# Performance work log

Measured on AMD Instinct MI355X. Metric: run time of the kernel, lower is better.

## Reference

```python
import jax, jax.numpy as jnp
from jax import lax
import numpy as np

MAX_VAL = 255.0
LEVELS = 5
MS_WEIGHTS = np.array([0.0448, 0.2856, 0.3001, 0.2363, 0.1333], dtype=np.float32)


def _gaussian_window(window_size: int, sigma: float) -> jnp.ndarray:
    # 1D gaussian -> outer product -> [1, 1, ws, ws] conv kernel (channel=1 depthwise)
    x = np.arange(window_size, dtype=np.float64)
    g = np.exp(-((x - window_size // 2) ** 2) / (2.0 * sigma ** 2))
    g = (g / g.sum()).astype(np.float32)
    w2d = np.outer(g, g)
    return jnp.asarray(w2d[None, None, :, :])


def _conv_same(x, win, pad):
    return lax.conv_general_dilated(
        x, win, window_strides=(1, 1), padding=[(pad, pad), (pad, pad)],
        dimension_numbers=('NCHW', 'OIHW', 'NCHW'))


def _ssim_level(img1, img2):
    _, _, w, h = img1.shape
    window_size = min(w, h, 11)
    sigma = 1.5 * window_size / 11
    win = _gaussian_window(window_size, sigma)
    pad = window_size // 2

    mu1 = _conv_same(img1, win, pad)
    mu2 = _conv_same(img2, win, pad)
    mu1_sq = mu1 * mu1
    mu2_sq = mu2 * mu2
    mu1_mu2 = mu1 * mu2
    sigma1_sq = _conv_same(img1 * img1, win, pad) - mu1_sq
    sigma2_sq = _conv_same(img2 * img2, win, pad) - mu2_sq
    sigma12 = _conv_same(img1 * img2, win, pad) - mu1_mu2

    C1 = (0.01 * MAX_VAL) ** 2
    C2 = (0.03 * MAX_VAL) ** 2
    V1 = 2.0 * sigma12 + C2
    V2 = sigma1_sq + sigma2_sq + C2
    ssim_map = (2.0 * mu1_mu2 + C1) * V1 / ((mu1_sq + mu2_sq + C1) * V2)
    mcs_map = V1 / V2
    return ssim_map.mean(), mcs_map.mean()


def _avg_pool2(x):
    b, c, h, w = x.shape
    return x.reshape(b, c, h // 2, 2, w // 2, 2).mean(axis=(3, 5))


def _ms_ssim(img1, img2):
    msssim = []
    mcs = []
    for _ in range(LEVELS):
        s, m = _ssim_level(img1, img2)
        msssim.append(s)
        mcs.append(m)
        img1 = _avg_pool2(img1)
        img2 = _avg_pool2(img2)
    weight = jnp.asarray(MS_WEIGHTS)
    mcs = jnp.stack(mcs)
    value = jnp.prod(mcs[:LEVELS - 1] ** weight[:LEVELS - 1]) * msssim[-1] ** weight[LEVELS - 1]
    return jnp.clip(value / 2.0, 0.0, 1.0)


def setup_inputs() -> dict:
    key = jax.random.key(0)
    k1, k2 = jax.random.split(key)
    shape = (16, 1, 512, 512)
    img1 = jax.random.uniform(k1, shape, dtype=jnp.float32)
    img2 = jax.random.uniform(k2, shape, dtype=jnp.float32)
    return {"img1": img1, "img2": img2}


def reference(img1, img2):
    return _ms_ssim(img1, img2)
```

## Files before the change

### kernel.cpp

```cpp
#include <hip/hip_runtime.h>
#include <math.h>


#define WS 11
#define TW 64
#define TH 32
#define SROWS 42
#define HSTRIDE 68

__global__ __launch_bounds__(256) void ssim_level_kernel(
    const float* __restrict__ img1, const float* __restrict__ img2,
    int H, int W,
    float* __restrict__ pool1, float* __restrict__ pool2,
    float* __restrict__ partials)
{
    __shared__ float hS[SROWS * HSTRIDE];
    __shared__ float hD[SROWS * HSTRIDE];
    __shared__ float hS2[SROWS * HSTRIDE];
    __shared__ float hD2[SROWS * HSTRIDE];
    __shared__ float wgs[WS];
    __shared__ float red[2][4];

    const int tid = threadIdx.x;

    if (tid == 0) {
        double g[WS]; double sum = 0.0;
        for (int i = 0; i < WS; ++i) {
            double d = (double)(i - 5);
            g[i] = exp(-(d * d) / 4.5);
            sum += g[i];
        }
        for (int i = 0; i < WS; ++i) wgs[i] = (float)(g[i] / sum);
    }
    __syncthreads();

    float w[WS];
#pragma unroll
    for (int j = 0; j < WS; ++j) w[j] = wgs[j];

    const int bx = blockIdx.x, by = blockIdx.y, b = blockIdx.z;
    const int x0 = bx * TW, y0 = by * TH;
    const float* p1 = img1 + (size_t)b * H * W;
    const float* p2 = img2 + (size_t)b * H * W;

#pragma unroll 1
    for (int t = tid; t < SROWS * 16; t += 256) {
        int r = t >> 4, xg = t & 15;
        int gy = y0 - 5 + r;
        int gxb = x0 - 8 + 4 * xg;
        float fs[20], fd[20];
        if (gy >= 0 && gy < H) {
            const float* r1p = p1 + (size_t)gy * W;
            const float* r2p = p2 + (size_t)gy * W;
#pragma unroll
            for (int k = 0; k < 5; ++k) {
                int gx = gxb + 4 * k;
                float4 a = make_float4(0.f, 0.f, 0.f, 0.f);
                float4 c = make_float4(0.f, 0.f, 0.f, 0.f);
                if (gx >= 0 && gx + 3 < W) {
                    a = *(const float4*)(r1p + gx);
                    c = *(const float4*)(r2p + gx);
                } else if (gx + 3 >= 0 && gx < W) {
                    float t1[4] = {0.f, 0.f, 0.f, 0.f};
                    float t2[4] = {0.f, 0.f, 0.f, 0.f};
#pragma unroll
                    for (int u = 0; u < 4; ++u) {
                        int gxx = gx + u;
                        if (gxx >= 0 && gxx < W) { t1[u] = r1p[gxx]; t2[u] = r2p[gxx]; }
                    }
                    a = make_float4(t1[0], t1[1], t1[2], t1[3]);
                    c = make_float4(t2[0], t2[1], t2[2], t2[3]);
                }
                fs[4 * k]     = a.x + c.x;  fd[4 * k]     = a.x - c.x;
                fs[4 * k + 1] = a.y + c.y;  fd[4 * k + 1] = a.y - c.y;
                fs[4 * k + 2] = a.z + c.z;  fd[4 * k + 2] = a.z - c.z;
                fs[4 * k + 3] = a.w + c.w;  fd[4 * k + 3] = a.w - c.w;
            }
        } else {
#pragma unroll
            for (int k = 0; k < 20; ++k) { fs[k] = 0.f; fd[k] = 0.f; }
        }
        float qs[14], qd[14];
#pragma unroll
        for (int k = 0; k < 14; ++k) {
            qs[k] = fs[k + 3] * fs[k + 3];
            qd[k] = fd[k + 3] * fd[k + 3];
        }
        float oS[4], oD[4], oS2[4], oD2[4];
#pragma unroll
        for (int c = 0; c < 4; ++c) {
            float aS = 0.f, aD = 0.f, aS2 = 0.f, aD2 = 0.f;
#pragma unroll
            for (int j = 0; j < WS; ++j) {
                float wj = w[j];
                aS  = fmaf(wj, fs[3 + c + j], aS);
                aD  = fmaf(wj, fd[3 + c + j], aD);
                aS2 = fmaf(wj, qs[c + j], aS2);
                aD2 = fmaf(wj, qd[c + j], aD2);
            }
            oS[c] = aS; oD[c] = aD; oS2[c] = aS2; oD2[c] = aD2;
        }
        int ho = r * HSTRIDE + 4 * xg;
        *(float4*)&hS[ho]  = make_float4(oS[0], oS[1], oS[2], oS[3]);
        *(float4*)&hD[ho]  = make_float4(oD[0], oD[1], oD[2], oD[3]);
        *(float4*)&hS2[ho] = make_float4(oS2[0], oS2[1], oS2[2], oS2[3]);
        *(float4*)&hD2[ho] = make_float4(oD2[0], oD2[1], oD2[2], oD2[3]);
    }

    if (pool1 != nullptr) {
        int pc = tid & 15, pr = tid >> 4;
        int Hp = H >> 1, Wp = W >> 1;
        int gy = y0 + 2 * pr, gx = x0 + 4 * pc;
        const float* r1a = p1 + (size_t)gy * W + gx;
        const float* r1b = r1a + W;
        const float* r2a = p2 + (size_t)gy * W + gx;
        const float* r2b = r2a + W;
        float4 a0 = *(const float4*)r1a, a1 = *(const float4*)r1b;
        float4 c0 = *(const float4*)r2a, c1 = *(const float4*)r2b;
        float2 px = make_float2(0.25f * (a0.x + a0.y + a1.x + a1.y),
                                0.25f * (a0.z + a0.w + a1.z + a1.w));
        float2 py = make_float2(0.25f * (c0.x + c0.y + c1.x + c1.y),
                                0.25f * (c0.z + c0.w + c1.z + c1.w));
        size_t o = ((size_t)b * Hp + (by * (TH / 2) + pr)) * Wp + (bx * (TW / 2) + 2 * pc);
        *(float2*)(pool1 + o) = px;
        *(float2*)(pool2 + o) = py;
    }

    __syncthreads();

    const int x = tid & 15;
    const int g = tid >> 4;
    float accS[2][4], accD[2][4], accS2[2][4], accD2[2][4];
#pragma unroll
    for (int rr = 0; rr < 2; ++rr)
#pragma unroll
        for (int c = 0; c < 4; ++c) {
            accS[rr][c] = 0.f; accD[rr][c] = 0.f;
            accS2[rr][c] = 0.f; accD2[rr][c] = 0.f;
        }

#pragma unroll
    for (int r = 0; r < 12; ++r) {
        int ho = (2 * g + r) * HSTRIDE + 4 * x;
        float4 vS  = *(const float4*)&hS[ho];
        float4 vD  = *(const float4*)&hD[ho];
        float4 vS2 = *(const float4*)&hS2[ho];
        float4 vD2 = *(const float4*)&hD2[ho];
        float lS[4] = {vS.x, vS.y, vS.z, vS.w};
        float lD[4] = {vD.x, vD.y, vD.z, vD.w};
        float lS2[4] = {vS2.x, vS2.y, vS2.z, vS2.w};
        float lD2[4] = {vD2.x, vD2.y, vD2.z, vD2.w};
        if (r < 11) {
            float wv = w[r];
#pragma unroll
            for (int c = 0; c < 4; ++c) {
                accS[0][c]  = fmaf(wv, lS[c],  accS[0][c]);
                accD[0][c]  = fmaf(wv, lD[c],  accD[0][c]);
                accS2[0][c] = fmaf(wv, lS2[c], accS2[0][c]);
                accD2[0][c] = fmaf(wv, lD2[c], accD2[0][c]);
            }
        }
        if (r >= 1) {
            float wv = w[r - 1];
#pragma unroll
            for (int c = 0; c < 4; ++c) {
                accS[1][c]  = fmaf(wv, lS[c],  accS[1][c]);
                accD[1][c]  = fmaf(wv, lD[c],  accD[1][c]);
                accS2[1][c] = fmaf(wv, lS2[c], accS2[1][c]);
                accD2[1][c] = fmaf(wv, lD2[c], accD2[1][c]);
            }
        }
    }

    const float C1 = 6.5025f;
    const float C2 = 58.5225f;
    const int Hv = min(TH, H - y0);
    const int Wv = min(TW, W - x0);
    float sacc = 0.f, macc = 0.f;
#pragma unroll
    for (int rr = 0; rr < 2; ++rr) {
        int row = 2 * g + rr;
#pragma unroll
        for (int c = 0; c < 4; ++c) {
            float ms = accS[rr][c], md = accD[rr][c];
            float es = accS2[rr][c], ed = accD2[rr][c];
            float ms2 = ms * ms, md2 = md * md;
            float a  = 0.5f * (ms2 - md2);
            float bb = 0.5f * (ms2 + md2);
            float pq = 0.5f * (es - ed);
            float qq = 0.5f * (es + ed);
            float V1 = (pq - a) + C2;
            float V2 = (qq - bb) + C2;
            float num = a + C1;
            float den = bb + C1;
            float inv = 1.0f / (den * V2);
            float sv = num * V1 * inv;
            float mv = V1 * den * inv;
            if (row < Hv && (4 * x + c) < Wv) { sacc += sv; macc += mv; }
        }
    }

#pragma unroll
    for (int o = 32; o > 0; o >>= 1) {
        sacc += __shfl_down(sacc, o);
        macc += __shfl_down(macc, o);
    }
    int wave = tid >> 6, lane = tid & 63;
    if (lane == 0) { red[0][wave] = sacc; red[1][wave] = macc; }
    __syncthreads();
    if (tid == 0) {
        float s = red[0][0] + red[0][1] + red[0][2] + red[0][3];
        float m = red[1][0] + red[1][1] + red[1][2] + red[1][3];
        size_t linear = ((size_t)blockIdx.z * gridDim.y + blockIdx.y) * gridDim.x + blockIdx.x;
        partials[2 * linear] = s;
        partials[2 * linear + 1] = m;
    }
}

__global__ __launch_bounds__(256) void finalize_kernel(
    const float* __restrict__ partials, float* __restrict__ out)
{
    __shared__ float lvl_s[5], lvl_m[5];
    __shared__ float red[2][4];
    const int nb[5] = {2048, 512, 128, 32, 16};
    const int off[5] = {0, 2048, 2560, 2688, 2720};
    const float npix[5] = {16.f * 512 * 512, 16.f * 256 * 256, 16.f * 128 * 128,
                           16.f * 64 * 64, 16.f * 32 * 32};
    const int tid = threadIdx.x;

    for (int l = 0; l < 5; ++l) {
        float s = 0.f, m = 0.f;
        for (int i = tid; i < nb[l]; i += 256) {
            s += partials[2 * (off[l] + i)];
            m += partials[2 * (off[l] + i) + 1];
        }
#pragma unroll
        for (int o = 32; o > 0; o >>= 1) {
            s += __shfl_down(s, o);
            m += __shfl_down(m, o);
        }
        int wave = tid >> 6, lane = tid & 63;
        if (lane == 0) { red[0][wave] = s; red[1][wave] = m; }
        __syncthreads();
        if (tid == 0) {
            lvl_s[l] = (red[0][0] + red[0][1] + red[0][2] + red[0][3]) / npix[l];
            lvl_m[l] = (red[1][0] + red[1][1] + red[1][2] + red[1][3]) / npix[l];
        }
        __syncthreads();
    }

    if (tid == 0) {
        const float w[5] = {0.0448f, 0.2856f, 0.3001f, 0.2363f, 0.1333f};
        float v = powf(lvl_m[0], w[0]) * powf(lvl_m[1], w[1]) * powf(lvl_m[2], w[2]) *
                  powf(lvl_m[3], w[3]) * powf(lvl_s[4], w[4]);
        v *= 0.5f;
        v = fminf(fmaxf(v, 0.f), 1.f);
        out[0] = v;
    }
}

extern "C" void kernel_launch(void* const* d_in, const int* in_sizes, int n_in,
                              void* d_out, int out_size, void* d_ws, size_t ws_size,
                              hipStream_t stream) {
    const float* img1 = (const float*)d_in[0];
    const float* img2 = (const float*)d_in[1];
    float* out = (float*)d_out;

    const int B = 16;

    float* wsf = (float*)d_ws;
    float* partials = wsf;
    float* p = wsf + 5472;
    float* p1_l1 = p; p += (size_t)B * 256 * 256;
    float* p2_l1 = p; p += (size_t)B * 256 * 256;
    float* p1_l2 = p; p += (size_t)B * 128 * 128;
    float* p2_l2 = p; p += (size_t)B * 128 * 128;
    float* p1_l3 = p; p += (size_t)B * 64 * 64;
    float* p2_l3 = p; p += (size_t)B * 64 * 64;
    float* p1_l4 = p; p += (size_t)B * 32 * 32;
    float* p2_l4 = p; p += (size_t)B * 32 * 32;

    const int part_off[5] = {0, 2048, 2560, 2688, 2720};

    dim3 block(256);

    ssim_level_kernel<<<dim3(8, 16, B), block, 0, stream>>>(
        img1, img2, 512, 512, p1_l1, p2_l1, partials + 2 * part_off[0]);
    ssim_level_kernel<<<dim3(4, 8, B), block, 0, stream>>>(
        p1_l1, p2_l1, 256, 256, p1_l2, p2_l2, partials + 2 * part_off[1]);
    ssim_level_kernel<<<dim3(2, 4, B), block, 0, stream>>>(
        p1_l2, p2_l2, 128, 128, p1_l3, p2_l3, partials + 2 * part_off[2]);
    ssim_level_kernel<<<dim3(1, 2, B), block, 0, stream>>>(
        p1_l3, p2_l3, 64, 64, p1_l4, p2_l4, partials + 2 * part_off[3]);
    ssim_level_kernel<<<dim3(1, 1, B), block, 0, stream>>>(
        p1_l4, p2_l4, 32, 32, nullptr, nullptr, partials + 2 * part_off[4]);

    finalize_kernel<<<1, block, 0, stream>>>(partials, out);
}
```

Measured before the change: 147.6 us.

## Build full pyramid in one pass and run all SSIM levels in one launch

A new kernel computes all four downsampled pyramid levels from 64x64 tiles of the full-resolution images, chaining the 2x2 pools through shared memory. A single SSIM kernel then handles every level, mapping a flat block index to a level and tile, so the five serial per-level launches with their tail effects become one launch where the small levels fill in beside the large one. Gaussian weights are now computed per thread in float instead of by one thread in double followed by a barrier. The cost is an extra full read of the input images for pooling and slight float differences in the weights.

```diff
diff --git a/kernel.cpp b/kernel.cpp
--- a/kernel.cpp
+++ b/kernel.cpp
@@ -8,40 +8,128 @@
 #define SROWS 42
 #define HSTRIDE 68
 
-__global__ __launch_bounds__(256) void ssim_level_kernel(
+__device__ __forceinline__ void gauss_weights(float* w) {
+    float s = 0.f;
+#pragma unroll
+    for (int j = 0; j < WS; ++j) {
+        float d = (float)(j - 5);
+        float e = expf(-d * d / 4.5f);
+        w[j] = e;
+        s += e;
+    }
+    float inv = 1.f / s;
+#pragma unroll
+    for (int j = 0; j < WS; ++j) w[j] *= inv;
+}
+
+__global__ __launch_bounds__(256) void pool_all_kernel(
     const float* __restrict__ img1, const float* __restrict__ img2,
-    int H, int W,
-    float* __restrict__ pool1, float* __restrict__ pool2,
+    float* __restrict__ l1a, float* __restrict__ l1b,
+    float* __restrict__ l2a, float* __restrict__ l2b,
+    float* __restrict__ l3a, float* __restrict__ l3b,
+    float* __restrict__ l4a, float* __restrict__ l4b)
+{
+    __shared__ float buf[64 * 68];
+    __shared__ float pl1[32 * 36];
+    __shared__ float pl2[16 * 20];
+    __shared__ float pl3[8 * 12];
+    const int tid = threadIdx.x;
+    const int rx = blockIdx.x, ry = blockIdx.y, b = blockIdx.z;
+    const int gx0 = rx * 64, gy0 = ry * 64;
+
+#pragma unroll 1
+    for (int q = 0; q < 2; ++q) {
+        const float* src = (q == 0 ? img1 : img2) + (size_t)b * 512 * 512;
+        float* d1 = (q == 0 ? l1a : l1b) + (size_t)b * 256 * 256;
+        float* d2 = (q == 0 ? l2a : l2b) + (size_t)b * 128 * 128;
+        float* d3 = (q == 0 ? l3a : l3b) + (size_t)b * 64 * 64;
+        float* d4 = (q == 0 ? l4a : l4b) + (size_t)b * 32 * 32;
+        if (q) __syncthreads();
+        for (int t = tid; t < 1024; t += 256) {
+            int r = t >> 4, c4 = t & 15;
+            float4 v = *(const float4*)(src + (size_t)(gy0 + r) * 512 + gx0 + 4 * c4);
+            *(float4*)&buf[r * 68 + 4 * c4] = v;
+        }
+        __syncthreads();
+        for (int t = tid; t < 1024; t += 256) {
+            int r = t >> 5, c = t & 31;
+            const float* p = &buf[(2 * r) * 68 + 2 * c];
+            float v = 0.25f * ((p[0] + p[1]) + (p[68] + p[69]));
+            pl1[r * 36 + c] = v;
+            d1[(size_t)(32 * ry + r) * 256 + 32 * rx + c] = v;
+        }
+        __syncthreads();
+        {
+            int r = tid >> 4, c = tid & 15;
+            const float* p = &pl1[(2 * r) * 36 + 2 * c];
+            float v = 0.25f * ((p[0] + p[1]) + (p[36] + p[37]));
+            pl2[r * 20 + c] = v;
+            d2[(size_t)(16 * ry + r) * 128 + 16 * rx + c] = v;
+        }
+        __syncthreads();
+        if (tid < 64) {
+            int r = tid >> 3, c = tid & 7;
+            const float* p = &pl2[(2 * r) * 20 + 2 * c];
+            float v = 0.25f * ((p[0] + p[1]) + (p[20] + p[21]));
+            pl3[r * 12 + c] = v;
+            d3[(size_t)(8 * ry + r) * 64 + 8 * rx + c] = v;
+        }
+        __syncthreads();
+        if (tid < 16) {
+            int r = tid >> 2, c = tid & 3;
+            const float* p = &pl3[(2 * r) * 12 + 2 * c];
+            float v = 0.25f * ((p[0] + p[1]) + (p[12] + p[13]));
+            d4[(size_t)(4 * ry + r) * 32 + 4 * rx + c] = v;
+        }
+    }
+}
+
+__global__ __launch_bounds__(256) void ssim_fused_kernel(
+    const float* __restrict__ img1, const float* __restrict__ img2,
+    const float* __restrict__ l1a, const float* __restrict__ l1b,
+    const float* __restrict__ l2a, const float* __restrict__ l2b,
+    const float* __restrict__ l3a, const float* __restrict__ l3b,
+    const float* __restrict__ l4a, const float* __restrict__ l4b,
     float* __restrict__ partials)
 {
     __shared__ float hS[SROWS * HSTRIDE];
     __shared__ float hD[SROWS * HSTRIDE];
     __shared__ float hS2[SROWS * HSTRIDE];
     __shared__ float hD2[SROWS * HSTRIDE];
-    __shared__ float wgs[WS];
     __shared__ float red[2][4];
 
     const int tid = threadIdx.x;
-
-    if (tid == 0) {
-        double g[WS]; double sum = 0.0;
-        for (int i = 0; i < WS; ++i) {
-            double d = (double)(i - 5);
-            g[i] = exp(-(d * d) / 4.5);
-            sum += g[i];
-        }
-        for (int i = 0; i < WS; ++i) wgs[i] = (float)(g[i] / sum);
-    }
-    __syncthreads();
+    const int lin = blockIdx.x;
+
+    int level, base;
+    if (lin < 2048)      { level = 0; base = 0; }
+    else if (lin < 2560) { level = 1; base = 2048; }
+    else if (lin < 2688) { level = 2; base = 2560; }
+    else if (lin < 2720) { level = 3; base = 2688; }
+    else                 { level = 4; base = 2720; }
+    const int Wt[5]   = {512, 256, 128, 64, 32};
+    const int ntxl[5] = {3, 2, 1, 0, 0};
+    const int ntyl[5] = {4, 3, 2, 1, 0};
+    const int W = Wt[level], H = W;
+    const int li = lin - base;
+    const int tx = li & ((1 << ntxl[level]) - 1);
+    const int rem = li >> ntxl[level];
+    const int ty = rem & ((1 << ntyl[level]) - 1);
+    const int b = rem >> ntyl[level];
+
+    const float* ip1; const float* ip2;
+    if (level == 0)      { ip1 = img1; ip2 = img2; }
+    else if (level == 1) { ip1 = l1a; ip2 = l1b; }
+    else if (level == 2) { ip1 = l2a; ip2 = l2b; }
+    else if (level == 3) { ip1 = l3a; ip2 = l3b; }
+    else                 { ip1 = l4a; ip2 = l4b; }
+    const float* p1 = ip1 + (size_t)b * H * W;
+    const float* p2 = ip2 + (size_t)b * H * W;
+
+    const int x0 = tx * TW, y0 = ty * TH;
 
     float w[WS];
-#pragma unroll
-    for (int j = 0; j < WS; ++j) w[j] = wgs[j];
-
-    const int bx = blockIdx.x, by = blockIdx.y, b = blockIdx.z;
-    const int x0 = bx * TW, y0 = by * TH;
-    const float* p1 = img1 + (size_t)b * H * W;
-    const float* p2 = img2 + (size_t)b * H * W;
+    gauss_weights(w);
 
 #pragma unroll 1
     for (int t = tid; t < SROWS * 16; t += 256) {
@@ -106,26 +194,6 @@
         *(float4*)&hS2[ho] = make_float4(oS2[0], oS2[1], oS2[2], oS2[3]);
         *(float4*)&hD2[ho] = make_float4(oD2[0], oD2[1], oD2[2], oD2[3]);
     }
-
-    if (pool1 != nullptr) {
-        int pc = tid & 15, pr = tid >> 4;
-        int Hp = H >> 1, Wp = W >> 1;
-        int gy = y0 + 2 * pr, gx = x0 + 4 * pc;
-        const float* r1a = p1 + (size_t)gy * W + gx;
-        const float* r1b = r1a + W;
-        const float* r2a = p2 + (size_t)gy * W + gx;
-        const float* r2b = r2a + W;
-        float4 a0 = *(const float4*)r1a, a1 = *(const float4*)r1b;
-        float4 c0 = *(const float4*)r2a, c1 = *(const float4*)r2b;
-        float2 px = make_float2(0.25f * (a0.x + a0.y + a1.x + a1.y),
-                                0.25f * (a0.z + a0.w + a1.z + a1.w));
-        float2 py = make_float2(0.25f * (c0.x + c0.y + c1.x + c1.y),
-                                0.25f * (c0.z + c0.w + c1.z + c1.w));
-        size_t o = ((size_t)b * Hp + (by * (TH / 2) + pr)) * Wp + (bx * (TW / 2) + 2 * pc);
-        *(float2*)(pool1 + o) = px;
-        *(float2*)(pool2 + o) = py;
-    }
-
     __syncthreads();
 
     const int x = tid & 15;
@@ -211,9 +279,8 @@
     if (tid == 0) {
         float s = red[0][0] + red[0][1] + red[0][2] + red[0][3];
         float m = red[1][0] + red[1][1] + red[1][2] + red[1][3];
-        size_t linear = ((size_t)blockIdx.z * gridDim.y + blockIdx.y) * gridDim.x + blockIdx.x;
-        partials[2 * linear] = s;
-        partials[2 * linear + 1] = m;
+        partials[2 * lin] = s;
+        partials[2 * lin + 1] = m;
     }
 }
 
@@ -271,29 +338,22 @@
     float* wsf = (float*)d_ws;
     float* partials = wsf;
     float* p = wsf + 5472;
-    float* p1_l1 = p; p += (size_t)B * 256 * 256;
-    float* p2_l1 = p; p += (size_t)B * 256 * 256;
-    float* p1_l2 = p; p += (size_t)B * 128 * 128;
-    float* p2_l2 = p; p += (size_t)B * 128 * 128;
-    float* p1_l3 = p; p += (size_t)B * 64 * 64;
-    float* p2_l3 = p; p += (size_t)B * 64 * 64;
-    float* p1_l4 = p; p += (size_t)B * 32 * 32;
-    float* p2_l4 = p; p += (size_t)B * 32 * 32;
-
-    const int part_off[5] = {0, 2048, 2560, 2688, 2720};
+    float* l1a = p; p += (size_t)B * 256 * 256;
+    float* l1b = p; p += (size_t)B * 256 * 256;
+    float* l2a = p; p += (size_t)B * 128 * 128;
+    float* l2b = p; p += (size_t)B * 128 * 128;
+    float* l3a = p; p += (size_t)B * 64 * 64;
+    float* l3b = p; p += (size_t)B * 64 * 64;
+    float* l4a = p; p += (size_t)B * 32 * 32;
+    float* l4b = p; p += (size_t)B * 32 * 32;
 
     dim3 block(256);
 
-    ssim_level_kernel<<<dim3(8, 16, B), block, 0, stream>>>(
-        img1, img2, 512, 512, p1_l1, p2_l1, partials + 2 * part_off[0]);
-    ssim_level_kernel<<<dim3(4, 8, B), block, 0, stream>>>(
-        p1_l1, p2_l1, 256, 256, p1_l2, p2_l2, partials + 2 * part_off[1]);
-    ssim_level_kernel<<<dim3(2, 4, B), block, 0, stream>>>(
-        p1_l2, p2_l2, 128, 128, p1_l3, p2_l3, partials + 2 * part_off[2]);
-    ssim_level_kernel<<<dim3(1, 2, B), block, 0, stream>>>(
-        p1_l3, p2_l3, 64, 64, p1_l4, p2_l4, partials + 2 * part_off[3]);
-    ssim_level_kernel<<<dim3(1, 1, B), block, 0, stream>>>(
-        p1_l4, p2_l4, 32, 32, nullptr, nullptr, partials + 2 * part_off[4]);
+    pool_all_kernel<<<dim3(8, 8, B), block, 0, stream>>>(
+        img1, img2, l1a, l1b, l2a, l2b, l3a, l3b, l4a, l4b);
+
+    ssim_fused_kernel<<<dim3(2736), block, 0, stream>>>(
+        img1, img2, l1a, l1b, l2a, l2b, l3a, l3b, l4a, l4b, partials);
 
     finalize_kernel<<<1, block, 0, stream>>>(partials, out);
 }
```

Result: faster. 129.4 us (-12.3%).

## Fuse all MS-SSIM levels and finalize into one kernel with on-the-fly pooling

Applied to the files above, without the earlier changes.

Replaces the five per-level launches plus the finalize launch with a single grid. Each block picks its pyramid level from its linear index and recomputes the pooled pixels directly from the full-resolution images into shared memory, using a templated recursive average. The last block to finish, detected with an atomic counter, reduces all partials and writes the result. This removes launch overhead and the serial dependency between levels, at the cost of redundant reads for deep levels (up to 256 loads per pooled pixel at level 4), more shared memory per block, and a memset launch.

```diff
diff --git a/kernel.cpp b/kernel.cpp
--- a/kernel.cpp
+++ b/kernel.cpp
@@ -7,78 +7,192 @@
 #define TH 32
 #define SROWS 42
 #define HSTRIDE 68
-
-__global__ __launch_bounds__(256) void ssim_level_kernel(
+#define PSTRIDE 84
+#define NBLK 2736
+
+__device__ __forceinline__ void gauss_weights(float* w) {
+    float s = 0.f;
+#pragma unroll
+    for (int j = 0; j < WS; ++j) {
+        float d = (float)(j - 5);
+        float e = expf(-d * d / 4.5f);
+        w[j] = e;
+        s += e;
+    }
+    float inv = 1.f / s;
+#pragma unroll
+    for (int j = 0; j < WS; ++j) w[j] *= inv;
+}
+
+template<int L>
+__device__ __forceinline__ float poolT(const float* __restrict__ img, int y, int x) {
+    if constexpr (L == 0) {
+        return img[(y << 9) + x];
+    } else {
+        return 0.25f * ((poolT<L-1>(img, 2*y, 2*x)   + poolT<L-1>(img, 2*y, 2*x+1)) +
+                        (poolT<L-1>(img, 2*y+1, 2*x) + poolT<L-1>(img, 2*y+1, 2*x+1)));
+    }
+}
+
+__global__ __launch_bounds__(256) void msssim_all_kernel(
     const float* __restrict__ img1, const float* __restrict__ img2,
-    int H, int W,
-    float* __restrict__ pool1, float* __restrict__ pool2,
-    float* __restrict__ partials)
+    float* __restrict__ partials, unsigned int* __restrict__ counter,
+    float* __restrict__ out)
 {
     __shared__ float hS[SROWS * HSTRIDE];
     __shared__ float hD[SROWS * HSTRIDE];
     __shared__ float hS2[SROWS * HSTRIDE];
     __shared__ float hD2[SROWS * HSTRIDE];
-    __shared__ float wgs[WS];
+    __shared__ float pS[SROWS * PSTRIDE];
+    __shared__ float pD[SROWS * PSTRIDE];
     __shared__ float red[2][4];
+    __shared__ int lastflag;
 
     const int tid = threadIdx.x;
-
-    if (tid == 0) {
-        double g[WS]; double sum = 0.0;
-        for (int i = 0; i < WS; ++i) {
-            double d = (double)(i - 5);
-            g[i] = exp(-(d * d) / 4.5);
-            sum += g[i];
-        }
-        for (int i = 0; i < WS; ++i) wgs[i] = (float)(g[i] / sum);
-    }
-    __syncthreads();
+    const int lin = blockIdx.x;
+
+    int level, li;
+    if (lin < 16)       { level = 4; li = lin; }
+    else if (lin < 48)  { level = 3; li = lin - 16; }
+    else if (lin < 176) { level = 2; li = lin - 48; }
+    else if (lin < 688) { level = 1; li = lin - 176; }
+    else                { level = 0; li = lin - 688; }
+
+    const int ntxl[5] = {3, 2, 1, 0, 0};
+    const int ntyl[5] = {4, 3, 2, 1, 0};
+    const int W = 512 >> level;
+    const int tx = li & ((1 << ntxl[level]) - 1);
+    const int rem = li >> ntxl[level];
+    const int ty = rem & ((1 << ntyl[level]) - 1);
+    const int b = rem >> ntyl[level];
+    const int x0 = tx * TW, y0 = ty * TH;
+
+    const float* p1 = img1 + (size_t)b * 512 * 512;
+    const float* p2 = img2 + (size_t)b * 512 * 512;
 
     float w[WS];
-#pragma unroll
-    for (int j = 0; j < WS; ++j) w[j] = wgs[j];
-
-    const int bx = blockIdx.x, by = blockIdx.y, b = blockIdx.z;
-    const int x0 = bx * TW, y0 = by * TH;
-    const float* p1 = img1 + (size_t)b * H * W;
-    const float* p2 = img2 + (size_t)b * H * W;
-
+    gauss_weights(w);
+
+    if (level > 0) {
+        if (level == 1) {
+            for (int t = tid; t < SROWS * 80; t += 256) {
+                int r = t / 80, c = t - r * 80;
+                int gy = y0 - 5 + r, gx = x0 - 8 + c;
+                float vS = 0.f, vD = 0.f;
+                if ((unsigned)gy < (unsigned)W && (unsigned)gx < (unsigned)W) {
+                    float a = poolT<1>(p1, gy, gx);
+                    float bb = poolT<1>(p2, gy, gx);
+                    vS = a + bb; vD = a - bb;
+                }
+                pS[r * PSTRIDE + c] = vS;
+                pD[r * PSTRIDE + c] = vD;
+            }
+        } else if (level == 2) {
+            for (int t = tid; t < SROWS * 80; t += 256) {
+                int r = t / 80, c = t - r * 80;
+                int gy = y0 - 5 + r, gx = x0 - 8 + c;
+                float vS = 0.f, vD = 0.f;
+                if ((unsigned)gy < (unsigned)W && (unsigned)gx < (unsigned)W) {
+                    float a = poolT<2>(p1, gy, gx);
+                    float bb = poolT<2>(p2, gy, gx);
+                    vS = a + bb; vD = a - bb;
+                }
+                pS[r * PSTRIDE + c] = vS;
+                pD[r * PSTRIDE + c] = vD;
+            }
+        } else if (level == 3) {
+            for (int t = tid; t < SROWS * 80; t += 256) {
+                int r = t / 80, c = t - r * 80;
+                int gy = y0 - 5 + r, gx = x0 - 8 + c;
+                float vS = 0.f, vD = 0.f;
+                if ((unsigned)gy < (unsigned)W && (unsigned)gx < (unsigned)W) {
+                    float a = poolT<3>(p1, gy, gx);
+                    float bb = poolT<3>(p2, gy, gx);
+                    vS = a + bb; vD = a - bb;
+                }
+                pS[r * PSTRIDE + c] = vS;
+                pD[r * PSTRIDE + c] = vD;
+            }
+        } else {
+            for (int t = tid; t < SROWS * 80; t += 256) {
+                int r = t / 80, c = t - r * 80;
+                int gy = y0 - 5 + r, gx = x0 - 8 + c;
+                float vS = 0.f, vD = 0.f;
+                if ((unsigned)gy < (unsigned)W && (unsigned)gx < (unsigned)W) {
+                    float a = poolT<4>(p1, gy, gx);
+                    float bb = poolT<4>(p2, gy, gx);
+                    vS = a + bb; vD = a - bb;
+                }
+                pS[r * PSTRIDE + c] = vS;
+                pD[r * PSTRIDE + c] = vD;
+            }
+        }
+        __syncthreads();
+    }
+
+    const bool interior = (level == 0) && (x0 >= 8) && (x0 <= 440) &&
+                          (y0 >= 5) && (y0 <= 475);
 #pragma unroll 1
     for (int t = tid; t < SROWS * 16; t += 256) {
         int r = t >> 4, xg = t & 15;
-        int gy = y0 - 5 + r;
-        int gxb = x0 - 8 + 4 * xg;
         float fs[20], fd[20];
-        if (gy >= 0 && gy < H) {
-            const float* r1p = p1 + (size_t)gy * W;
-            const float* r2p = p2 + (size_t)gy * W;
+        if (level == 0) {
+            int gy = y0 - 5 + r;
+            int gxb = x0 - 8 + 4 * xg;
+            if (interior) {
+                const float* r1p = p1 + (size_t)gy * 512 + gxb;
+                const float* r2p = p2 + (size_t)gy * 512 + gxb;
+#pragma unroll
+                for (int k = 0; k < 5; ++k) {
+                    float4 a = *(const float4*)(r1p + 4 * k);
+                    float4 c = *(const float4*)(r2p + 4 * k);
+                    fs[4 * k]     = a.x + c.x;  fd[4 * k]     = a.x - c.x;
+                    fs[4 * k + 1] = a.y + c.y;  fd[4 * k + 1] = a.y - c.y;
+                    fs[4 * k + 2] = a.z + c.z;  fd[4 * k + 2] = a.z - c.z;
+                    fs[4 * k + 3] = a.w + c.w;  fd[4 * k + 3] = a.w - c.w;
+                }
+            } else if (gy >= 0 && gy < 512) {
+                const float* r1p = p1 + (size_t)gy * 512;
+                const float* r2p = p2 + (size_t)gy * 512;
+#pragma unroll
+                for (int k = 0; k < 5; ++k) {
+                    int gx = gxb + 4 * k;
+                    float4 a = make_float4(0.f, 0.f, 0.f, 0.f);
+                    float4 c = make_float4(0.f, 0.f, 0.f, 0.f);
+                    if (gx >= 0 && gx + 3 < 512) {
+                        a = *(const float4*)(r1p + gx);
+                        c = *(const float4*)(r2p + gx);
+                    } else if (gx + 3 >= 0 && gx < 512) {
+                        float t1[4] = {0.f, 0.f, 0.f, 0.f};
+                        float t2[4] = {0.f, 0.f, 0.f, 0.f};
+#pragma unroll
+                        for (int u = 0; u < 4; ++u) {
+                            int gxx = gx + u;
+                            if (gxx >= 0 && gxx < 512) { t1[u] = r1p[gxx]; t2[u] = r2p[gxx]; }
+                        }
+                        a = make_float4(t1[0], t1[1], t1[2], t1[3]);
+                        c = make_float4(t2[0], t2[1], t2[2], t2[3]);
+                    }
+                    fs[4 * k]     = a.x + c.x;  fd[4 * k]     = a.x - c.x;
+                    fs[4 * k + 1] = a.y + c.y;  fd[4 * k + 1] = a.y - c.y;
+                    fs[4 * k + 2] = a.z + c.z;  fd[4 * k + 2] = a.z - c.z;
+                    fs[4 * k + 3] = a.w + c.w;  fd[4 * k + 3] = a.w - c.w;
+                }
+            } else {
+#pragma unroll
+                for (int k = 0; k < 20; ++k) { fs[k] = 0.f; fd[k] = 0.f; }
+            }
+        } else {
+            int base = r * PSTRIDE + 4 * xg;
 #pragma unroll
             for (int k = 0; k < 5; ++k) {
-                int gx = gxb + 4 * k;
-                float4 a = make_float4(0.f, 0.f, 0.f, 0.f);
-                float4 c = make_float4(0.f, 0.f, 0.f, 0.f);
-                if (gx >= 0 && gx + 3 < W) {
-                    a = *(const float4*)(r1p + gx);
-                    c = *(const float4*)(r2p + gx);
-                } else if (gx + 3 >= 0 && gx < W) {
-                    float t1[4] = {0.f, 0.f, 0.f, 0.f};
-                    float t2[4] = {0.f, 0.f, 0.f, 0.f};
-#pragma unroll
-                    for (int u = 0; u < 4; ++u) {
-                        int gxx = gx + u;
-                        if (gxx >= 0 && gxx < W) { t1[u] = r1p[gxx]; t2[u] = r2p[gxx]; }
-                    }
-                    a = make_float4(t1[0], t1[1], t1[2], t1[3]);
-                    c = make_float4(t2[0], t2[1], t2[2], t2[3]);
-                }
-                fs[4 * k]     = a.x + c.x;  fd[4 * k]     = a.x - c.x;
-                fs[4 * k + 1] = a.y + c.y;  fd[4 * k + 1] = a.y - c.y;
-                fs[4 * k + 2] = a.z + c.z;  fd[4 * k + 2] = a.z - c.z;
-                fs[4 * k + 3] = a.w + c.w;  fd[4 * k + 3] = a.w - c.w;
-            }
-        } else {
-#pragma unroll
-            for (int k = 0; k < 20; ++k) { fs[k] = 0.f; fd[k] = 0.f; }
+                float4 a = *(const float4*)&pS[base + 4 * k];
+                float4 c = *(const float4*)&pD[base + 4 * k];
+                fs[4 * k]     = a.x;  fd[4 * k]     = c.x;
+                fs[4 * k + 1] = a.y;  fd[4 * k + 1] = c.y;
+                fs[4 * k + 2] = a.z;  fd[4 * k + 2] = c.z;
+                fs[4 * k + 3] = a.w;  fd[4 * k + 3] = c.w;
+            }
         }
         float qs[14], qd[14];
 #pragma unroll
@@ -106,26 +220,6 @@
         *(float4*)&hS2[ho] = make_float4(oS2[0], oS2[1], oS2[2], oS2[3]);
         *(float4*)&hD2[ho] = make_float4(oD2[0], oD2[1], oD2[2], oD2[3]);
     }
-
-    if (pool1 != nullptr) {
-        int pc = tid & 15, pr = tid >> 4;
-        int Hp = H >> 1, Wp = W >> 1;
-        int gy = y0 + 2 * pr, gx = x0 + 4 * pc;
-        const float* r1a = p1 + (size_t)gy * W + gx;
-        const float* r1b = r1a + W;
-        const float* r2a = p2 + (size_t)gy * W + gx;
-        const float* r2b = r2a + W;
-        float4 a0 = *(const float4*)r1a, a1 = *(const float4*)r1b;
-        float4 c0 = *(const float4*)r2a, c1 = *(const float4*)r2b;
-        float2 px = make_float2(0.25f * (a0.x + a0.y + a1.x + a1.y),
-                                0.25f * (a0.z + a0.w + a1.z + a1.w));
-        float2 py = make_float2(0.25f * (c0.x + c0.y + c1.x + c1.y),
-                                0.25f * (c0.z + c0.w + c1.z + c1.w));
-        size_t o = ((size_t)b * Hp + (by * (TH / 2) + pr)) * Wp + (bx * (TW / 2) + 2 * pc);
-        *(float2*)(pool1 + o) = px;
-        *(float2*)(pool2 + o) = py;
-    }
-
     __syncthreads();
 
     const int x = tid & 15;
@@ -174,7 +268,7 @@
 
     const float C1 = 6.5025f;
     const float C2 = 58.5225f;
-    const int Hv = min(TH, H - y0);
+    const int Hv = min(TH, W - y0);
     const int Wv = min(TW, W - x0);
     float sacc = 0.f, macc = 0.f;
 #pragma unroll
@@ -211,51 +305,62 @@
     if (tid == 0) {
         float s = red[0][0] + red[0][1] + red[0][2] + red[0][3];
         float m = red[1][0] + red[1][1] + red[1][2] + red[1][3];
-        size_t linear = ((size_t)blockIdx.z * gridDim.y + blockIdx.y) * gridDim.x + blockIdx.x;
-        partials[2 * linear] = s;
-        partials[2 * linear + 1] = m;
-    }
-}
-
-__global__ __launch_bounds__(256) void finalize_kernel(
-    const float* __restrict__ partials, float* __restrict__ out)
-{
-    __shared__ float lvl_s[5], lvl_m[5];
-    __shared__ float red[2][4];
-    const int nb[5] = {2048, 512, 128, 32, 16};
-    const int off[5] = {0, 2048, 2560, 2688, 2720};
-    const float npix[5] = {16.f * 512 * 512, 16.f * 256 * 256, 16.f * 128 * 128,
-                           16.f * 64 * 64, 16.f * 32 * 32};
-    const int tid = threadIdx.x;
-
-    for (int l = 0; l < 5; ++l) {
-        float s = 0.f, m = 0.f;
-        for (int i = tid; i < nb[l]; i += 256) {
-            s += partials[2 * (off[l] + i)];
-            m += partials[2 * (off[l] + i) + 1];
+        partials[2 * lin] = s;
+        partials[2 * lin + 1] = m;
+        __threadfence();
+        unsigned int old = __hip_atomic_fetch_add(counter, 1u, __ATOMIC_ACQ_REL,
+                                                  __HIP_MEMORY_SCOPE_AGENT);
+        lastflag = (old == NBLK - 1) ? 1 : 0;
+    }
+    __syncthreads();
+
+    if (lastflag) {
+        __threadfence();
+        const int offk[5] = {0, 16, 48, 176, 688};
+        const int endk[5] = {16, 48, 176, 688, NBLK};
+        float aS[5], aM[5];
+#pragma unroll
+        for (int k = 0; k < 5; ++k) {
+            float s = 0.f, m = 0.f;
+            for (int i = offk[k] + tid; i < endk[k]; i += 256) {
+                s += partials[2 * i];
+                m += partials[2 * i + 1];
+            }
+            aS[k] = s; aM[k] = m;
         }
 #pragma unroll
         for (int o = 32; o > 0; o >>= 1) {
-            s += __shfl_down(s, o);
-            m += __shfl_down(m, o);
-        }
-        int wave = tid >> 6, lane = tid & 63;
-        if (lane == 0) { red[0][wave] = s; red[1][wave] = m; }
+#pragma unroll
+            for (int k = 0; k < 5; ++k) {
+                aS[k] += __shfl_down(aS[k], o);
+                aM[k] += __shfl_down(aM[k], o);
+            }
+        }
+        if (lane == 0) {
+#pragma unroll
+            for (int k = 0; k < 5; ++k) {
+                pS[wave * 16 + k] = aS[k];
+                pS[wave * 16 + 8 + k] = aM[k];
+            }
+        }
         __syncthreads();
         if (tid == 0) {
-            lvl_s[l] = (red[0][0] + red[0][1] + red[0][2] + red[0][3]) / npix[l];
-            lvl_m[l] = (red[1][0] + red[1][1] + red[1][2] + red[1][3]) / npix[l];
-        }
-        __syncthreads();
-    }
-
-    if (tid == 0) {
-        const float w[5] = {0.0448f, 0.2856f, 0.3001f, 0.2363f, 0.1333f};
-        float v = powf(lvl_m[0], w[0]) * powf(lvl_m[1], w[1]) * powf(lvl_m[2], w[2]) *
-                  powf(lvl_m[3], w[3]) * powf(lvl_s[4], w[4]);
-        v *= 0.5f;
-        v = fminf(fmaxf(v, 0.f), 1.f);
-        out[0] = v;
+            const float npix[5] = {16384.f, 65536.f, 262144.f, 1048576.f, 4194304.f};
+            float ls[5], lm[5];
+#pragma unroll
+            for (int k = 0; k < 5; ++k) {
+                float s = pS[k] + pS[16 + k] + pS[32 + k] + pS[48 + k];
+                float m = pS[8 + k] + pS[24 + k] + pS[40 + k] + pS[56 + k];
+                ls[k] = s / npix[k];
+                lm[k] = m / npix[k];
+            }
+            const float wt[5] = {0.0448f, 0.2856f, 0.3001f, 0.2363f, 0.1333f};
+            float v = powf(lm[4], wt[0]) * powf(lm[3], wt[1]) * powf(lm[2], wt[2]) *
+                      powf(lm[1], wt[3]) * powf(ls[0], wt[4]);
+            v *= 0.5f;
+            v = fminf(fmaxf(v, 0.f), 1.f);
+            out[0] = v;
+        }
     }
 }
 
@@ -266,34 +371,12 @@
     const float* img2 = (const float*)d_in[1];
     float* out = (float*)d_out;
 
-    const int B = 16;
-
     float* wsf = (float*)d_ws;
     float* partials = wsf;
-    float* p = wsf + 5472;
-    float* p1_l1 = p; p += (size_t)B * 256 * 256;
-    float* p2_l1 = p; p += (size_t)B * 256 * 256;
-    float* p1_l2 = p; p += (size_t)B * 128 * 128;
-    float* p2_l2 = p; p += (size_t)B * 128 * 128;
-    float* p1_l3 = p; p += (size_t)B * 64 * 64;
-    float* p2_l3 = p; p += (size_t)B * 64 * 64;
-    float* p1_l4 = p; p += (size_t)B * 32 * 32;
-    float* p2_l4 = p; p += (size_t)B * 32 * 32;
-
-    const int part_off[5] = {0, 2048, 2560, 2688, 2720};
-
-    dim3 block(256);
-
-    ssim_level_kernel<<<dim3(8, 16, B), block, 0, stream>>>(
-        img1, img2, 512, 512, p1_l1, p2_l1, partials + 2 * part_off[0]);
-    ssim_level_kernel<<<dim3(4, 8, B), block, 0, stream>>>(
-        p1_l1, p2_l1, 256, 256, p1_l2, p2_l2, partials + 2 * part_off[1]);
-    ssim_level_kernel<<<dim3(2, 4, B), block, 0, stream>>>(
-        p1_l2, p2_l2, 128, 128, p1_l3, p2_l3, partials + 2 * part_off[2]);
-    ssim_level_kernel<<<dim3(1, 2, B), block, 0, stream>>>(
-        p1_l3, p2_l3, 64, 64, p1_l4, p2_l4, partials + 2 * part_off[3]);
-    ssim_level_kernel<<<dim3(1, 1, B), block, 0, stream>>>(
-        p1_l4, p2_l4, 32, 32, nullptr, nullptr, partials + 2 * part_off[4]);
-
-    finalize_kernel<<<1, block, 0, stream>>>(partials, out);
+    unsigned int* counter = (unsigned int*)(wsf + 2 * NBLK);
+
+    hipMemsetAsync(counter, 0, sizeof(unsigned int), stream);
+
+    msssim_all_kernel<<<dim3(NBLK), dim3(256), 0, stream>>>(
+        img1, img2, partials, counter, out);
 }
```

Measured after the change: 263.6 us. 1.79x slower.
